# Optimization experiments

Measured on AMD Instinct MI355X. Metric: run time of the kernel, lower is better.

The kernel has to match this reference:

```python
import jax, jax.numpy as jnp
import numpy as np

A, B, T, N, C = 8, 4, 1024, 4, 2048
EPS = 1e-5
SINKHORN_ITERS = 20


def setup_inputs() -> dict:
    key = jax.random.key(0)
    ks = jax.random.split(key, 8)
    nC = N * C
    # identity-ish init per module, with small random alphas to exercise all paths
    p = 1.0 / N
    inv_sig = float(np.log(p) - np.log(1.0 - p))
    return {
        "x": jax.random.normal(ks[0], (B, T, N, C), dtype=jnp.float32),
        "output": jax.random.normal(ks[1], (B, T, C), dtype=jnp.float32),
        "input_norm_weight": jnp.ones((A, nC), dtype=jnp.float32),
        "phi_pre": 0.02 * jax.random.normal(ks[2], (A, nC, N), dtype=jnp.float32),
        "phi_post": 0.02 * jax.random.normal(ks[3], (A, nC, N), dtype=jnp.float32),
        "phi_res": 0.02 * jax.random.normal(ks[4], (A, nC, N * N), dtype=jnp.float32),
        "b_pre": jnp.full((A, N), inv_sig, dtype=jnp.float32),
        "b_post": jnp.zeros((A, N), dtype=jnp.float32),
        "b_res": jnp.broadcast_to(10.0 * jnp.eye(N, dtype=jnp.float32), (A, N, N)),
        "alpha_pre": 0.1 * jax.random.normal(ks[5], (A,), dtype=jnp.float32),
        "alpha_post": 0.1 * jax.random.normal(ks[6], (A,), dtype=jnp.float32),
        "alpha_res": 0.1 * jax.random.normal(ks[7], (A,), dtype=jnp.float32),
        "adapter_indices": jax.random.randint(jax.random.fold_in(key, 99), (B,), 0, A, dtype=jnp.int32),
    }


def sinkhorn_knopp(logits, iters):
    # logits: (B,T,n,n) -> doubly-stochastic M via alternating row/col normalization
    M = jnp.exp(logits)
    for _ in range(iters):
        M = M / M.sum(axis=-1, keepdims=True)
        M = M / M.sum(axis=-2, keepdims=True)
    return M


def reference(x, output, input_norm_weight, phi_pre, phi_post, phi_res,
              b_pre, b_post, b_res, alpha_pre, alpha_post, alpha_res,
              adapter_indices):
    Bs, Ts, n, Cc = x.shape
    idx = adapter_indices
    # per-sample adapter gather
    w = input_norm_weight[idx]                      # (B, n*C)
    x_flat = x.reshape(Bs, Ts, n * Cc)              # (B, T, n*C)
    rms = jnp.sqrt(jnp.mean(x_flat * x_flat, axis=-1, keepdims=True) + EPS)
    x_norm = w[:, None, :] * x_flat / rms           # (B, T, n*C)
    # pre gating
    pre_logits = jnp.einsum('btf,bfn->btn', x_norm, phi_pre[idx])
    H_pre = jax.nn.sigmoid(alpha_pre[idx][:, None, None] * pre_logits + b_pre[idx][:, None, :])
    x_agg = jnp.einsum('btn,btnc->btc', H_pre, x)   # (B, T, C)
    # post gating
    post_logits = jnp.einsum('btf,bfn->btn', x_norm, phi_post[idx])
    H_post = 2.0 * jax.nn.sigmoid(alpha_post[idx][:, None, None] * post_logits + b_post[idx][:, None, :])
    # residual mixing matrix via Sinkhorn
    res_logits = jnp.einsum('btf,bfm->btm', x_norm, phi_res[idx]).reshape(Bs, Ts, n, n)
    tilde_res = alpha_res[idx][:, None, None, None] * res_logits + b_res[idx][:, None, :, :]
    M = sinkhorn_knopp(tilde_res, SINKHORN_ITERS)   # (B, T, n, n)
    x_mixed = jnp.einsum('btij,btjc->btic', M, x)   # (B, T, n, C)
    y_dist = H_post[..., None] * output[:, :, None, :]
    out = x_mixed + y_dist                          # (B, T, n, C)
    return x_agg, out
```

## Files before the change

kernel.cpp:

```cpp
#include <hip/hip_runtime.h>

#define EPS 1e-5f
#define TOKS 4096
#define NCF 8192
#define CCH 2048
#define PHI_T_BYTES ((size_t)8 * 32 * 8192 * 2)
#define GATES_OFF PHI_T_BYTES
#define WS_NEED (PHI_T_BYTES + (size_t)TOKS * 32 * 4)

typedef __attribute__((ext_vector_type(8))) short bf16x8;
typedef __attribute__((ext_vector_type(4))) float f32x4;

__device__ __forceinline__ unsigned short f2bf(float f) {
  unsigned int u = __float_as_uint(f);
  u += 0x7FFFu + ((u >> 16) & 1u);
  return (unsigned short)(u >> 16);
}
__device__ __forceinline__ float bf2f(unsigned short s) {
  return __uint_as_float(((unsigned int)s) << 16);
}

__global__ __launch_bounds__(256)
void prep_phiT(const float* __restrict__ pre, const float* __restrict__ post,
               const float* __restrict__ res, unsigned short* __restrict__ phiT) {
  const int gid = blockIdx.x * 256 + threadIdx.x;
  const int a = gid >> 15;
  const int r = (gid >> 10) & 31;
  const int f = (gid & 1023) * 8;
  unsigned int w[4];
  #pragma unroll
  for (int p = 0; p < 4; ++p) {
    float v0 = 0.f, v1 = 0.f;
    const int e0 = f + 2 * p, e1 = f + 2 * p + 1;
    if (r < 4) {
      v0 = pre[((size_t)a * NCF + e0) * 4 + r];
      v1 = pre[((size_t)a * NCF + e1) * 4 + r];
    } else if (r < 8) {
      v0 = post[((size_t)a * NCF + e0) * 4 + (r - 4)];
      v1 = post[((size_t)a * NCF + e1) * 4 + (r - 4)];
    } else if (r < 24) {
      v0 = res[((size_t)a * NCF + e0) * 16 + (r - 8)];
      v1 = res[((size_t)a * NCF + e1) * 16 + (r - 8)];
    }
    w[p] = (unsigned int)f2bf(v0) | ((unsigned int)f2bf(v1) << 16);
  }
  *(uint4*)(phiT + ((size_t)a * 32 + r) * NCF + f) = make_uint4(w[0], w[1], w[2], w[3]);
}

__global__ __launch_bounds__(512, 1)
void logits_gates(const float* __restrict__ x,
                  const float* __restrict__ wnorm,
                  const unsigned short* __restrict__ phiT,
                  const float* __restrict__ b_pre, const float* __restrict__ b_post,
                  const float* __restrict__ b_res,
                  const float* __restrict__ a_pre, const float* __restrict__ a_post,
                  const float* __restrict__ a_res,
                  const int* __restrict__ aidx_arr,
                  float* __restrict__ gates) {
  __shared__ unsigned short xs[8][16 * 264];
  __shared__ float logits_s[8][16][32];
  __shared__ float ssq_s[8][16];

  const int tid = threadIdx.x;
  const int wave = tid >> 6, lane = tid & 63;
  const int tok0 = blockIdx.x * 16;
  const int aidx = aidx_arr[tok0 >> 10];
  const int kbase = wave * 1024;

  const float* xbase = x + (size_t)tok0 * NCF + kbase + lane * 4;
  const float* wbase = wnorm + (size_t)aidx * NCF + kbase + lane * 4;
  const unsigned short* pBbase =
      phiT + ((size_t)aidx * 32 + (lane & 15)) * NCF + kbase + (lane >> 4) * 8;

  f32x4 acc0 = {0.f, 0.f, 0.f, 0.f};
  f32x4 acc1 = {0.f, 0.f, 0.f, 0.f};
  float ssq[16];
  #pragma unroll
  for (int r = 0; r < 16; ++r) ssq[r] = 0.f;

  float4 xr[16];
  #pragma unroll
  for (int r = 0; r < 16; ++r) xr[r] = *(const float4*)(xbase + (size_t)r * NCF);

  for (int t = 0; t < 4; ++t) {
    const float4 wv = *(const float4*)(wbase + t * 256);
    #pragma unroll
    for (int r = 0; r < 16; ++r) {
      const float4 xv = xr[r];
      ssq[r] += xv.x * xv.x + xv.y * xv.y + xv.z * xv.z + xv.w * xv.w;
      ushort4 u = make_ushort4(f2bf(xv.x * wv.x), f2bf(xv.y * wv.y),
                               f2bf(xv.z * wv.z), f2bf(xv.w * wv.w));
      *(ushort4*)&xs[wave][r * 264 + lane * 4] = u;
    }
    if (t < 3) {
      #pragma unroll
      for (int r = 0; r < 16; ++r)
        xr[r] = *(const float4*)(xbase + (size_t)r * NCF + (t + 1) * 256);
    }
    const unsigned short* pB = pBbase + t * 256;
    #pragma unroll
    for (int s = 0; s < 8; ++s) {
      bf16x8 a = *(const bf16x8*)&xs[wave][(lane & 15) * 264 + s * 32 + (lane >> 4) * 8];
      bf16x8 b0 = *(const bf16x8*)(pB + s * 32);
      bf16x8 b1 = *(const bf16x8*)(pB + 16 * NCF + s * 32);
      acc0 = __builtin_amdgcn_mfma_f32_16x16x32_bf16(a, b0, acc0, 0, 0, 0);
      acc1 = __builtin_amdgcn_mfma_f32_16x16x32_bf16(a, b1, acc1, 0, 0, 0);
    }
  }

  #pragma unroll
  for (int r = 0; r < 16; ++r) {
    float v = ssq[r];
    #pragma unroll
    for (int m = 1; m <= 32; m <<= 1) v += __shfl_xor(v, m, 64);
    if (lane == 0) ssq_s[wave][r] = v;
  }
  #pragma unroll
  for (int i = 0; i < 4; ++i) {
    logits_s[wave][(lane >> 4) * 4 + i][lane & 15] = acc0[i];
    logits_s[wave][(lane >> 4) * 4 + i][16 + (lane & 15)] = acc1[i];
  }
  __syncthreads();

  if (tid < 256) {
    const int tok = tid >> 4, cl = tid & 15;
    float L0 = 0.f, L16 = 0.f, ssqt = 0.f;
    #pragma unroll
    for (int w = 0; w < 8; ++w) {
      L0 += logits_s[w][tok][cl];
      L16 += logits_s[w][tok][16 + cl];
      ssqt += ssq_s[w][tok];
    }
    const float invr = rsqrtf(ssqt * (1.f / NCF) + EPS);

    float* g = gates + (size_t)(tok0 + tok) * 32;
    if (cl < 4) {
      const float zp = a_pre[aidx] * L0 * invr + b_pre[(size_t)aidx * 4 + cl];
      g[cl] = 1.f / (1.f + __expf(-zp));
    } else if (cl < 8) {
      const float zq = a_post[aidx] * L0 * invr + b_post[(size_t)aidx * 4 + (cl - 4)];
      g[cl] = 2.f / (1.f + __expf(-zq));
    }
    const float resv = __shfl_xor((cl & 8) ? L0 : L16, 8, 64);
    const float tl = a_res[aidx] * resv * invr + b_res[(size_t)aidx * 16 + cl];
    float m = __expf(tl);
    #pragma unroll
    for (int it = 0; it < 20; ++it) {
      float rs = m;
      rs += __shfl_xor(rs, 1, 64);
      rs += __shfl_xor(rs, 2, 64);
      m *= __builtin_amdgcn_rcpf(rs);
      float cs = m;
      cs += __shfl_xor(cs, 4, 64);
      cs += __shfl_xor(cs, 8, 64);
      m *= __builtin_amdgcn_rcpf(cs);
    }
    g[8 + cl] = m;
  }
}

__global__ __launch_bounds__(256)
void out_pass(const float* __restrict__ x, const float* __restrict__ outp,
              const float* __restrict__ gates,
              float* __restrict__ agg, float* __restrict__ big) {
  const int tok = blockIdx.x;
  const int tid = threadIdx.x;
  const float* g = gates + (size_t)tok * 32;
  float hp[4], hq[4], M[16];
  #pragma unroll
  for (int i = 0; i < 4; ++i) { hp[i] = g[i]; hq[i] = g[4 + i]; }
  #pragma unroll
  for (int i = 0; i < 16; ++i) M[i] = g[8 + i];

  const float* xrow = x + (size_t)tok * NCF;
  const float* orow = outp + (size_t)tok * CCH;
  float* arow = agg + (size_t)tok * CCH;
  float* brow = big + (size_t)tok * NCF;

  #pragma unroll
  for (int rep = 0; rep < 2; ++rep) {
    const int c = rep * 1024 + tid * 4;
    float4 xv[4];
    #pragma unroll
    for (int j = 0; j < 4; ++j) xv[j] = *(const float4*)(xrow + j * CCH + c);
    const float4 ov = *(const float4*)(orow + c);

    f32x4 ag;
    ag.x = hp[0]*xv[0].x + hp[1]*xv[1].x + hp[2]*xv[2].x + hp[3]*xv[3].x;
    ag.y = hp[0]*xv[0].y + hp[1]*xv[1].y + hp[2]*xv[2].y + hp[3]*xv[3].y;
    ag.z = hp[0]*xv[0].z + hp[1]*xv[1].z + hp[2]*xv[2].z + hp[3]*xv[3].z;
    ag.w = hp[0]*xv[0].w + hp[1]*xv[1].w + hp[2]*xv[2].w + hp[3]*xv[3].w;
    __builtin_nontemporal_store(ag, (f32x4*)(arow + c));

    #pragma unroll
    for (int i = 0; i < 4; ++i) {
      const float m0 = M[i*4+0], m1 = M[i*4+1], m2 = M[i*4+2], m3 = M[i*4+3];
      f32x4 o;
      o.x = m0*xv[0].x + m1*xv[1].x + m2*xv[2].x + m3*xv[3].x + hq[i]*ov.x;
      o.y = m0*xv[0].y + m1*xv[1].y + m2*xv[2].y + m3*xv[3].y + hq[i]*ov.y;
      o.z = m0*xv[0].z + m1*xv[1].z + m2*xv[2].z + m3*xv[3].z + hq[i]*ov.z;
      o.w = m0*xv[0].w + m1*xv[1].w + m2*xv[2].w + m3*xv[3].w + hq[i]*ov.w;
      __builtin_nontemporal_store(o, (f32x4*)(brow + i * CCH + c));
    }
  }
}

__global__ __launch_bounds__(256, 4)
void lora_fused(const float* __restrict__ x, const float* __restrict__ outp,
                const float* __restrict__ wnorm, const float* __restrict__ phi_pre,
                const float* __restrict__ phi_post, const float* __restrict__ phi_res,
                const float* __restrict__ b_pre, const float* __restrict__ b_post,
                const float* __restrict__ b_res, const float* __restrict__ a_pre,
                const float* __restrict__ a_post, const float* __restrict__ a_res,
                const int* __restrict__ aidx_arr, float* __restrict__ agg_out,
                float* __restrict__ big_out) {
  __shared__ unsigned short xsb[2][NCF];
  __shared__ float scratch[4][52];
  __shared__ float red[52];
  __shared__ float Hpre[2][4], Hpost[2][4], Msm[2][16];
  const int tid = threadIdx.x;
  const int tok0 = blockIdx.x * 2;
  const int aidx = aidx_arr[tok0 >> 10];
  const float* xr0 = x + (size_t)tok0 * NCF;
  const float* xr1 = xr0 + NCF;
  const float* wr = wnorm + (size_t)aidx * NCF;
  const float* pp = phi_pre + (size_t)aidx * NCF * 4;
  const float* pq = phi_post + (size_t)aidx * NCF * 4;
  const float* pr = phi_res + (size_t)aidx * NCF * 16;
  float acc[50];
  #pragma unroll
  for (int i = 0; i < 50; ++i) acc[i] = 0.f;
  for (int k = 0; k < 8; ++k) {
    const int f0 = (k * 256 + tid) * 4;
    const float4 w4 = *(const float4*)(wr + f0);
    const float4 xa = *(const float4*)(xr0 + f0);
    const float4 xb = *(const float4*)(xr1 + f0);
    acc[0] += xa.x*xa.x + xa.y*xa.y + xa.z*xa.z + xa.w*xa.w;
    acc[25] += xb.x*xb.x + xb.y*xb.y + xb.z*xb.z + xb.w*xb.w;
    float xw0[4] = { xa.x*w4.x, xa.y*w4.y, xa.z*w4.z, xa.w*w4.w };
    float xw1[4] = { xb.x*w4.x, xb.y*w4.y, xb.z*w4.z, xb.w*w4.w };
    *(ushort4*)&xsb[0][f0] = make_ushort4(f2bf(xa.x), f2bf(xa.y), f2bf(xa.z), f2bf(xa.w));
    *(ushort4*)&xsb[1][f0] = make_ushort4(f2bf(xb.x), f2bf(xb.y), f2bf(xb.z), f2bf(xb.w));
    #pragma unroll
    for (int d = 0; d < 4; ++d) {
      const int f = f0 + d;
      const float a0 = xw0[d], a1 = xw1[d];
      float col[24];
      const float4 P = *(const float4*)(pp + ((size_t)f << 2));
      const float4 Q = *(const float4*)(pq + ((size_t)f << 2));
      const float4 R0 = *(const float4*)(pr + ((size_t)f << 4));
      const float4 R1 = *(const float4*)(pr + ((size_t)f << 4) + 4);
      const float4 R2 = *(const float4*)(pr + ((size_t)f << 4) + 8);
      const float4 R3 = *(const float4*)(pr + ((size_t)f << 4) + 12);
      col[0]=P.x; col[1]=P.y; col[2]=P.z; col[3]=P.w;
      col[4]=Q.x; col[5]=Q.y; col[6]=Q.z; col[7]=Q.w;
      col[8]=R0.x; col[9]=R0.y; col[10]=R0.z; col[11]=R0.w;
      col[12]=R1.x; col[13]=R1.y; col[14]=R1.z; col[15]=R1.w;
      col[16]=R2.x; col[17]=R2.y; col[18]=R2.z; col[19]=R2.w;
      col[20]=R3.x; col[21]=R3.y; col[22]=R3.z; col[23]=R3.w;
      #pragma unroll
      for (int c = 0; c < 24; ++c) { acc[1 + c] += a0 * col[c]; acc[26 + c] += a1 * col[c]; }
    }
  }
  #pragma unroll
  for (int m = 1; m <= 32; m <<= 1) {
    #pragma unroll
    for (int v = 0; v < 50; ++v) acc[v] += __shfl_xor(acc[v], m, 64);
  }
  const int wave = tid >> 6, lane = tid & 63;
  if (lane == 0) {
    #pragma unroll
    for (int v = 0; v < 50; ++v) scratch[wave][v] = acc[v];
  }
  __syncthreads();
  if (tid < 50) red[tid] = scratch[0][tid] + scratch[1][tid] + scratch[2][tid] + scratch[3][tid];
  __syncthreads();
  if (tid < 32) {
    const int t = tid >> 4, l = tid & 15;
    const float invr = rsqrtf(red[t * 25] * (1.f / NCF) + EPS);
    const float tl = a_res[aidx] * red[t * 25 + 1 + 8 + l] * invr + b_res[(size_t)aidx * 16 + l];
    float m = __expf(tl);
    #pragma unroll
    for (int it = 0; it < 20; ++it) {
      float rs = m; rs += __shfl_xor(rs, 1, 64); rs += __shfl_xor(rs, 2, 64);
      m *= __builtin_amdgcn_rcpf(rs);
      float cs = m; cs += __shfl_xor(cs, 4, 64); cs += __shfl_xor(cs, 8, 64);
      m *= __builtin_amdgcn_rcpf(cs);
    }
    Msm[t][l] = m;
  } else if (tid < 40) {
    const int q = tid - 32, t = q >> 2, n = q & 3;
    const float invr = rsqrtf(red[t * 25] * (1.f / NCF) + EPS);
    const float zp = a_pre[aidx] * red[t * 25 + 1 + n] * invr + b_pre[(size_t)aidx * 4 + n];
    const float zq = a_post[aidx] * red[t * 25 + 1 + 4 + n] * invr + b_post[(size_t)aidx * 4 + n];
    Hpre[t][n] = 1.f / (1.f + __expf(-zp));
    Hpost[t][n] = 2.f / (1.f + __expf(-zq));
  }
  __syncthreads();
  #pragma unroll
  for (int t = 0; t < 2; ++t) {
    const int tok = tok0 + t;
    const float* orow = outp + (size_t)tok * CCH;
    float* arow = agg_out + (size_t)tok * CCH;
    float* brow = big_out + (size_t)tok * 4 * CCH;
    const float hp0 = Hpre[t][0], hp1 = Hpre[t][1], hp2 = Hpre[t][2], hp3 = Hpre[t][3];
    float Mr[16];
    #pragma unroll
    for (int i = 0; i < 16; ++i) Mr[i] = Msm[t][i];
    const float hq[4] = { Hpost[t][0], Hpost[t][1], Hpost[t][2], Hpost[t][3] };
    #pragma unroll
    for (int w = 0; w < 2; ++w) {
      const int c0 = (w * 256 + tid) * 4;
      float4 xv[4];
      #pragma unroll
      for (int n = 0; n < 4; ++n) {
        const ushort4 u = *(const ushort4*)&xsb[t][n * CCH + c0];
        xv[n] = make_float4(bf2f(u.x), bf2f(u.y), bf2f(u.z), bf2f(u.w));
      }
      const float4 ov = *(const float4*)(orow + c0);
      float4 ag;
      ag.x = hp0*xv[0].x + hp1*xv[1].x + hp2*xv[2].x + hp3*xv[3].x;
      ag.y = hp0*xv[0].y + hp1*xv[1].y + hp2*xv[2].y + hp3*xv[3].y;
      ag.z = hp0*xv[0].z + hp1*xv[1].z + hp2*xv[2].z + hp3*xv[3].z;
      ag.w = hp0*xv[0].w + hp1*xv[1].w + hp2*xv[2].w + hp3*xv[3].w;
      *(float4*)(arow + c0) = ag;
      #pragma unroll
      for (int i = 0; i < 4; ++i) {
        const float m0 = Mr[i*4+0], m1 = Mr[i*4+1], m2 = Mr[i*4+2], m3 = Mr[i*4+3];
        float4 o;
        o.x = m0*xv[0].x + m1*xv[1].x + m2*xv[2].x + m3*xv[3].x + hq[i]*ov.x;
        o.y = m0*xv[0].y + m1*xv[1].y + m2*xv[2].y + m3*xv[3].y + hq[i]*ov.y;
        o.z = m0*xv[0].z + m1*xv[1].z + m2*xv[2].z + m3*xv[3].z + hq[i]*ov.z;
        o.w = m0*xv[0].w + m1*xv[1].w + m2*xv[2].w + m3*xv[3].w + hq[i]*ov.w;
        *(float4*)(brow + (size_t)i * CCH + c0) = o;
      }
    }
  }
}

extern "C" void kernel_launch(void* const* d_in, const int* in_sizes, int n_in,
                              void* d_out, int out_size, void* d_ws, size_t ws_size,
                              hipStream_t stream) {
  const float* x     = (const float*)d_in[0];
  const float* outp  = (const float*)d_in[1];
  const float* wnorm = (const float*)d_in[2];
  const float* ppre  = (const float*)d_in[3];
  const float* ppost = (const float*)d_in[4];
  const float* pres  = (const float*)d_in[5];
  const float* bpre  = (const float*)d_in[6];
  const float* bpost = (const float*)d_in[7];
  const float* bres  = (const float*)d_in[8];
  const float* apre  = (const float*)d_in[9];
  const float* apost = (const float*)d_in[10];
  const float* ares  = (const float*)d_in[11];
  const int*   aidx  = (const int*)d_in[12];

  float* agg = (float*)d_out;
  float* big = (float*)d_out + (size_t)TOKS * CCH;

  if (ws_size >= WS_NEED) {
    unsigned short* phiT = (unsigned short*)d_ws;
    float* gates = (float*)((char*)d_ws + GATES_OFF);
    hipLaunchKernelGGL(prep_phiT, dim3(1024), dim3(256), 0, stream, ppre, ppost, pres, phiT);
    hipLaunchKernelGGL(logits_gates, dim3(256), dim3(512), 0, stream,
                       x, wnorm, phiT, bpre, bpost, bres, apre, apost, ares, aidx, gates);
    hipLaunchKernelGGL(out_pass, dim3(4096), dim3(256), 0, stream, x, outp, gates, agg, big);
  } else {
    hipLaunchKernelGGL(lora_fused, dim3(2048), dim3(256), 0, stream,
                       x, outp, wnorm, ppre, ppost, pres,
                       bpre, bpost, bres, apre, apost, ares, aidx, agg, big);
  }
}
```

Measured before the change: 100.7 us.

## Fuse gate computation and output pass, keep x tile in registers as bf16

Merges the logits/gates kernel and the output kernel into one kernel, so x is read from global memory once instead of twice. The gates stay in shared memory. Each thread keeps its x slice as packed bf16 in registers and reuses it for the aggregate and mixed outputs. The RMS-norm weight is folded into the transposed phi during prep, and waves now split the work by channel slice across the four streams. The cost is lower output precision (x is rounded to bf16 before mixing), heavy register pressure with possible spills, and only one large block per CU during the store-heavy phase.

After: 159.6 us. 58.5% more time.

```diff
diff --git a/kernel.cpp b/kernel.cpp
--- a/kernel.cpp
+++ b/kernel.cpp
@@ -4,9 +4,7 @@
 #define TOKS 4096
 #define NCF 8192
 #define CCH 2048
-#define PHI_T_BYTES ((size_t)8 * 32 * 8192 * 2)
-#define GATES_OFF PHI_T_BYTES
-#define WS_NEED (PHI_T_BYTES + (size_t)TOKS * 32 * 4)
+#define WS_NEED ((size_t)8 * 32 * 8192 * 2)
 
 typedef __attribute__((ext_vector_type(8))) short bf16x8;
 typedef __attribute__((ext_vector_type(4))) float f32x4;
@@ -22,11 +20,15 @@
 
 __global__ __launch_bounds__(256)
 void prep_phiT(const float* __restrict__ pre, const float* __restrict__ post,
-               const float* __restrict__ res, unsigned short* __restrict__ phiT) {
+               const float* __restrict__ res, const float* __restrict__ wnorm,
+               unsigned short* __restrict__ phiT) {
   const int gid = blockIdx.x * 256 + threadIdx.x;
   const int a = gid >> 15;
   const int r = (gid >> 10) & 31;
   const int f = (gid & 1023) * 8;
+  const float4 wA = *(const float4*)(wnorm + (size_t)a * NCF + f);
+  const float4 wB = *(const float4*)(wnorm + (size_t)a * NCF + f + 4);
+  const float wv[8] = { wA.x, wA.y, wA.z, wA.w, wB.x, wB.y, wB.z, wB.w };
   unsigned int w[4];
   #pragma unroll
   for (int p = 0; p < 4; ++p) {
@@ -42,35 +44,37 @@
       v0 = res[((size_t)a * NCF + e0) * 16 + (r - 8)];
       v1 = res[((size_t)a * NCF + e1) * 16 + (r - 8)];
     }
+    v0 *= wv[2 * p];
+    v1 *= wv[2 * p + 1];
     w[p] = (unsigned int)f2bf(v0) | ((unsigned int)f2bf(v1) << 16);
   }
   *(uint4*)(phiT + ((size_t)a * 32 + r) * NCF + f) = make_uint4(w[0], w[1], w[2], w[3]);
 }
 
-__global__ __launch_bounds__(512, 1)
-void logits_gates(const float* __restrict__ x,
-                  const float* __restrict__ wnorm,
+__global__ __launch_bounds__(512)
+void lora_fused16(const float* __restrict__ x,
+                  const float* __restrict__ outp,
                   const unsigned short* __restrict__ phiT,
                   const float* __restrict__ b_pre, const float* __restrict__ b_post,
                   const float* __restrict__ b_res,
                   const float* __restrict__ a_pre, const float* __restrict__ a_post,
                   const float* __restrict__ a_res,
                   const int* __restrict__ aidx_arr,
-                  float* __restrict__ gates) {
+                  float* __restrict__ agg, float* __restrict__ big) {
   __shared__ unsigned short xs[8][16 * 264];
   __shared__ float logits_s[8][16][32];
   __shared__ float ssq_s[8][16];
+  __shared__ float gates_s[16][24];
 
   const int tid = threadIdx.x;
   const int wave = tid >> 6, lane = tid & 63;
   const int tok0 = blockIdx.x * 16;
   const int aidx = aidx_arr[tok0 >> 10];
-  const int kbase = wave * 1024;
-
-  const float* xbase = x + (size_t)tok0 * NCF + kbase + lane * 4;
-  const float* wbase = wnorm + (size_t)aidx * NCF + kbase + lane * 4;
+  const int cbase = wave * 256 + lane * 4;
+
+  const float* xbase = x + (size_t)tok0 * NCF + cbase;
   const unsigned short* pBbase =
-      phiT + ((size_t)aidx * 32 + (lane & 15)) * NCF + kbase + (lane >> 4) * 8;
+      phiT + ((size_t)aidx * 32 + (lane & 15)) * NCF + wave * 256 + (lane >> 4) * 8;
 
   f32x4 acc0 = {0.f, 0.f, 0.f, 0.f};
   f32x4 acc1 = {0.f, 0.f, 0.f, 0.f};
@@ -78,26 +82,28 @@
   #pragma unroll
   for (int r = 0; r < 16; ++r) ssq[r] = 0.f;
 
+  uint2 xsav[16][4];
+
   float4 xr[16];
   #pragma unroll
   for (int r = 0; r < 16; ++r) xr[r] = *(const float4*)(xbase + (size_t)r * NCF);
 
-  for (int t = 0; t < 4; ++t) {
-    const float4 wv = *(const float4*)(wbase + t * 256);
+  for (int n = 0; n < 4; ++n) {
     #pragma unroll
     for (int r = 0; r < 16; ++r) {
-      const float4 xv = xr[r];
-      ssq[r] += xv.x * xv.x + xv.y * xv.y + xv.z * xv.z + xv.w * xv.w;
-      ushort4 u = make_ushort4(f2bf(xv.x * wv.x), f2bf(xv.y * wv.y),
-                               f2bf(xv.z * wv.z), f2bf(xv.w * wv.w));
-      *(ushort4*)&xs[wave][r * 264 + lane * 4] = u;
-    }
-    if (t < 3) {
+      const float4 v = xr[r];
+      ssq[r] += v.x * v.x + v.y * v.y + v.z * v.z + v.w * v.w;
+      const unsigned int lo = (unsigned int)f2bf(v.x) | ((unsigned int)f2bf(v.y) << 16);
+      const unsigned int hi = (unsigned int)f2bf(v.z) | ((unsigned int)f2bf(v.w) << 16);
+      xsav[r][n] = make_uint2(lo, hi);
+      *(uint2*)&xs[wave][r * 264 + lane * 4] = make_uint2(lo, hi);
+    }
+    if (n < 3) {
       #pragma unroll
       for (int r = 0; r < 16; ++r)
-        xr[r] = *(const float4*)(xbase + (size_t)r * NCF + (t + 1) * 256);
-    }
-    const unsigned short* pB = pBbase + t * 256;
+        xr[r] = *(const float4*)(xbase + (size_t)r * NCF + (n + 1) * 2048);
+    }
+    const unsigned short* pB = pBbase + n * 2048;
     #pragma unroll
     for (int s = 0; s < 8; ++s) {
       bf16x8 a = *(const bf16x8*)&xs[wave][(lane & 15) * 264 + s * 32 + (lane >> 4) * 8];
@@ -133,13 +139,12 @@
     }
     const float invr = rsqrtf(ssqt * (1.f / NCF) + EPS);
 
-    float* g = gates + (size_t)(tok0 + tok) * 32;
     if (cl < 4) {
       const float zp = a_pre[aidx] * L0 * invr + b_pre[(size_t)aidx * 4 + cl];
-      g[cl] = 1.f / (1.f + __expf(-zp));
+      gates_s[tok][cl] = 1.f / (1.f + __expf(-zp));
     } else if (cl < 8) {
       const float zq = a_post[aidx] * L0 * invr + b_post[(size_t)aidx * 4 + (cl - 4)];
-      g[cl] = 2.f / (1.f + __expf(-zq));
+      gates_s[tok][cl] = 2.f / (1.f + __expf(-zq));
     }
     const float resv = __shfl_xor((cl & 8) ? L0 : L16, 8, 64);
     const float tl = a_res[aidx] * resv * invr + b_res[(size_t)aidx * 16 + cl];
@@ -155,52 +160,48 @@
       cs += __shfl_xor(cs, 8, 64);
       m *= __builtin_amdgcn_rcpf(cs);
     }
-    g[8 + cl] = m;
-  }
-}
-
-__global__ __launch_bounds__(256)
-void out_pass(const float* __restrict__ x, const float* __restrict__ outp,
-              const float* __restrict__ gates,
-              float* __restrict__ agg, float* __restrict__ big) {
-  const int tok = blockIdx.x;
-  const int tid = threadIdx.x;
-  const float* g = gates + (size_t)tok * 32;
-  float hp[4], hq[4], M[16];
-  #pragma unroll
-  for (int i = 0; i < 4; ++i) { hp[i] = g[i]; hq[i] = g[4 + i]; }
-  #pragma unroll
-  for (int i = 0; i < 16; ++i) M[i] = g[8 + i];
-
-  const float* xrow = x + (size_t)tok * NCF;
-  const float* orow = outp + (size_t)tok * CCH;
-  float* arow = agg + (size_t)tok * CCH;
-  float* brow = big + (size_t)tok * NCF;
-
-  #pragma unroll
-  for (int rep = 0; rep < 2; ++rep) {
-    const int c = rep * 1024 + tid * 4;
-    float4 xv[4];
-    #pragma unroll
-    for (int j = 0; j < 4; ++j) xv[j] = *(const float4*)(xrow + j * CCH + c);
-    const float4 ov = *(const float4*)(orow + c);
+    gates_s[tok][8 + cl] = m;
+  }
+  __syncthreads();
+
+  #pragma unroll
+  for (int r = 0; r < 16; ++r) {
+    const int gtok = tok0 + r;
+    const float hp0 = gates_s[r][0], hp1 = gates_s[r][1],
+                hp2 = gates_s[r][2], hp3 = gates_s[r][3];
+    const float hq[4] = { gates_s[r][4], gates_s[r][5], gates_s[r][6], gates_s[r][7] };
+    float M[16];
+    #pragma unroll
+    for (int i = 0; i < 16; ++i) M[i] = gates_s[r][8 + i];
+
+    float4 xw[4];
+    #pragma unroll
+    for (int j = 0; j < 4; ++j) {
+      const uint2 p = xsav[r][j];
+      xw[j] = make_float4(bf2f((unsigned short)(p.x & 0xffff)),
+                          bf2f((unsigned short)(p.x >> 16)),
+                          bf2f((unsigned short)(p.y & 0xffff)),
+                          bf2f((unsigned short)(p.y >> 16)));
+    }
+    const float4 ov = *(const float4*)(outp + (size_t)gtok * CCH + cbase);
 
     f32x4 ag;
-    ag.x = hp[0]*xv[0].x + hp[1]*xv[1].x + hp[2]*xv[2].x + hp[3]*xv[3].x;
-    ag.y = hp[0]*xv[0].y + hp[1]*xv[1].y + hp[2]*xv[2].y + hp[3]*xv[3].y;
-    ag.z = hp[0]*xv[0].z + hp[1]*xv[1].z + hp[2]*xv[2].z + hp[3]*xv[3].z;
-    ag.w = hp[0]*xv[0].w + hp[1]*xv[1].w + hp[2]*xv[2].w + hp[3]*xv[3].w;
-    __builtin_nontemporal_store(ag, (f32x4*)(arow + c));
-
+    ag.x = hp0*xw[0].x + hp1*xw[1].x + hp2*xw[2].x + hp3*xw[3].x;
+    ag.y = hp0*xw[0].y + hp1*xw[1].y + hp2*xw[2].y + hp3*xw[3].y;
+    ag.z = hp0*xw[0].z + hp1*xw[1].z + hp2*xw[2].z + hp3*xw[3].z;
+    ag.w = hp0*xw[0].w + hp1*xw[1].w + hp2*xw[2].w + hp3*xw[3].w;
+    __builtin_nontemporal_store(ag, (f32x4*)(agg + (size_t)gtok * CCH + cbase));
+
+    float* brow = big + (size_t)gtok * NCF + cbase;
     #pragma unroll
     for (int i = 0; i < 4; ++i) {
       const float m0 = M[i*4+0], m1 = M[i*4+1], m2 = M[i*4+2], m3 = M[i*4+3];
       f32x4 o;
-      o.x = m0*xv[0].x + m1*xv[1].x + m2*xv[2].x + m3*xv[3].x + hq[i]*ov.x;
-      o.y = m0*xv[0].y + m1*xv[1].y + m2*xv[2].y + m3*xv[3].y + hq[i]*ov.y;
-      o.z = m0*xv[0].z + m1*xv[1].z + m2*xv[2].z + m3*xv[3].z + hq[i]*ov.z;
-      o.w = m0*xv[0].w + m1*xv[1].w + m2*xv[2].w + m3*xv[3].w + hq[i]*ov.w;
-      __builtin_nontemporal_store(o, (f32x4*)(brow + i * CCH + c));
+      o.x = m0*xw[0].x + m1*xw[1].x + m2*xw[2].x + m3*xw[3].x + hq[i]*ov.x;
+      o.y = m0*xw[0].y + m1*xw[1].y + m2*xw[2].y + m3*xw[3].y + hq[i]*ov.y;
+      o.z = m0*xw[0].z + m1*xw[1].z + m2*xw[2].z + m3*xw[3].z + hq[i]*ov.z;
+      o.w = m0*xw[0].w + m1*xw[1].w + m2*xw[2].w + m3*xw[3].w + hq[i]*ov.w;
+      __builtin_nontemporal_store(o, (f32x4*)(brow + (size_t)i * CCH));
     }
   }
 }
@@ -360,11 +361,10 @@
 
   if (ws_size >= WS_NEED) {
     unsigned short* phiT = (unsigned short*)d_ws;
-    float* gates = (float*)((char*)d_ws + GATES_OFF);
-    hipLaunchKernelGGL(prep_phiT, dim3(1024), dim3(256), 0, stream, ppre, ppost, pres, phiT);
-    hipLaunchKernelGGL(logits_gates, dim3(256), dim3(512), 0, stream,
-                       x, wnorm, phiT, bpre, bpost, bres, apre, apost, ares, aidx, gates);
-    hipLaunchKernelGGL(out_pass, dim3(4096), dim3(256), 0, stream, x, outp, gates, agg, big);
+    hipLaunchKernelGGL(prep_phiT, dim3(1024), dim3(256), 0, stream,
+                       ppre, ppost, pres, wnorm, phiT);
+    hipLaunchKernelGGL(lora_fused16, dim3(256), dim3(512), 0, stream,
+                       x, outp, phiT, bpre, bpost, bres, apre, apost, ares, aidx, agg, big);
   } else {
     hipLaunchKernelGGL(lora_fused, dim3(2048), dim3(256), 0, stream,
                        x, outp, wnorm, ppre, ppost, pres,
```

## Split logits GEMM over K into two blocks and fold norm weight into phi

Applied to the files above, without the earlier changes.

The logits kernel is split into two blocks per 16-token tile, each covering half of the feature dimension. Each block writes partial logits and sum-of-squares to workspace, and a new small kernel reduces them and computes the gates and Sinkhorn. The per-adapter RMSNorm weight is premultiplied into the bf16 phi matrix during prep, which removes a load and multiply from the hot loop. This doubles the grid and allows higher occupancy, at the cost of an extra launch and a workspace round trip for the partials.

Measured after the change: 149.8 us. 48.7% more time.

```diff
diff --git a/kernel.cpp b/kernel.cpp
--- a/kernel.cpp
+++ b/kernel.cpp
@@ -4,9 +4,12 @@
 #define TOKS 4096
 #define NCF 8192
 #define CCH 2048
-#define PHI_T_BYTES ((size_t)8 * 32 * 8192 * 2)
-#define GATES_OFF PHI_T_BYTES
-#define WS_NEED (PHI_T_BYTES + (size_t)TOKS * 32 * 4)
+
+#define PHI_BYTES ((size_t)8 * 32 * 8192 * 2)
+#define LOGP_OFF  PHI_BYTES
+#define SSQP_OFF  (LOGP_OFF + (size_t)512 * 16 * 32 * 4)
+#define GATES_OFF (SSQP_OFF + (size_t)512 * 16 * 4)
+#define WS_NEED   (GATES_OFF + (size_t)TOKS * 32 * 4)
 
 typedef __attribute__((ext_vector_type(8))) short bf16x8;
 typedef __attribute__((ext_vector_type(4))) float f32x4;
@@ -22,11 +25,15 @@
 
 __global__ __launch_bounds__(256)
 void prep_phiT(const float* __restrict__ pre, const float* __restrict__ post,
-               const float* __restrict__ res, unsigned short* __restrict__ phiT) {
+               const float* __restrict__ res, const float* __restrict__ wnorm,
+               unsigned short* __restrict__ phiT) {
   const int gid = blockIdx.x * 256 + threadIdx.x;
   const int a = gid >> 15;
   const int r = (gid >> 10) & 31;
   const int f = (gid & 1023) * 8;
+  const float4 wA = *(const float4*)(wnorm + (size_t)a * NCF + f);
+  const float4 wB = *(const float4*)(wnorm + (size_t)a * NCF + f + 4);
+  const float wv[8] = { wA.x, wA.y, wA.z, wA.w, wB.x, wB.y, wB.z, wB.w };
   unsigned int w[4];
   #pragma unroll
   for (int p = 0; p < 4; ++p) {
@@ -42,121 +49,129 @@
       v0 = res[((size_t)a * NCF + e0) * 16 + (r - 8)];
       v1 = res[((size_t)a * NCF + e1) * 16 + (r - 8)];
     }
+    v0 *= wv[2 * p];
+    v1 *= wv[2 * p + 1];
     w[p] = (unsigned int)f2bf(v0) | ((unsigned int)f2bf(v1) << 16);
   }
   *(uint4*)(phiT + ((size_t)a * 32 + r) * NCF + f) = make_uint4(w[0], w[1], w[2], w[3]);
 }
 
-__global__ __launch_bounds__(512, 1)
-void logits_gates(const float* __restrict__ x,
-                  const float* __restrict__ wnorm,
-                  const unsigned short* __restrict__ phiT,
+__global__ __launch_bounds__(512, 4)
+void logits_partial(const float* __restrict__ x,
+                    const unsigned short* __restrict__ phiT,
+                    const int* __restrict__ aidx_arr,
+                    float* __restrict__ logP,
+                    float* __restrict__ ssqP) {
+  __shared__ unsigned short xs[8][16 * 264];
+  __shared__ float logAcc[16][32];
+  __shared__ float ssqAcc[16];
+
+  const int tid = threadIdx.x;
+  const int wave = tid >> 6, lane = tid & 63;
+  const int tile = blockIdx.x >> 1;
+  const int h = blockIdx.x & 1;
+  const int tok0 = tile * 16;
+  const int koff = h * 4096;
+  const int aidx = aidx_arr[tok0 >> 10];
+
+  if (tid < 512) logAcc[tid >> 5][tid & 31] = 0.f;
+  if (tid < 16) ssqAcc[tid] = 0.f;
+  __syncthreads();
+
+  const float* xbase = x + (size_t)tok0 * NCF + koff + wave * 512 + lane * 4;
+  const unsigned short* pBbase =
+      phiT + ((size_t)aidx * 32 + (lane & 15)) * NCF + koff + wave * 512 + (lane >> 4) * 8;
+
+  f32x4 acc0 = {0.f, 0.f, 0.f, 0.f};
+  f32x4 acc1 = {0.f, 0.f, 0.f, 0.f};
+  float ssq[16];
+  #pragma unroll
+  for (int r = 0; r < 16; ++r) ssq[r] = 0.f;
+
+  for (int t = 0; t < 2; ++t) {
+    float4 xv[16];
+    #pragma unroll
+    for (int r = 0; r < 16; ++r)
+      xv[r] = *(const float4*)(xbase + (size_t)r * NCF + t * 256);
+    #pragma unroll
+    for (int r = 0; r < 16; ++r) {
+      const float4 v = xv[r];
+      ssq[r] += v.x * v.x + v.y * v.y + v.z * v.z + v.w * v.w;
+      *(ushort4*)&xs[wave][r * 264 + lane * 4] =
+          make_ushort4(f2bf(v.x), f2bf(v.y), f2bf(v.z), f2bf(v.w));
+    }
+    const unsigned short* pB = pBbase + t * 256;
+    #pragma unroll
+    for (int s = 0; s < 8; ++s) {
+      bf16x8 a = *(const bf16x8*)&xs[wave][(lane & 15) * 264 + s * 32 + (lane >> 4) * 8];
+      bf16x8 b0 = *(const bf16x8*)(pB + s * 32);
+      bf16x8 b1 = *(const bf16x8*)(pB + 16 * NCF + s * 32);
+      acc0 = __builtin_amdgcn_mfma_f32_16x16x32_bf16(a, b0, acc0, 0, 0, 0);
+      acc1 = __builtin_amdgcn_mfma_f32_16x16x32_bf16(a, b1, acc1, 0, 0, 0);
+    }
+  }
+
+  #pragma unroll
+  for (int r = 0; r < 16; ++r) {
+    float v = ssq[r];
+    #pragma unroll
+    for (int m = 1; m <= 32; m <<= 1) v += __shfl_xor(v, m, 64);
+    if (lane == 0) atomicAdd(&ssqAcc[r], v);
+  }
+  #pragma unroll
+  for (int i = 0; i < 4; ++i) {
+    atomicAdd(&logAcc[(lane >> 4) * 4 + i][lane & 15], acc0[i]);
+    atomicAdd(&logAcc[(lane >> 4) * 4 + i][16 + (lane & 15)], acc1[i]);
+  }
+  __syncthreads();
+
+  if (tid < 512) logP[(size_t)blockIdx.x * 512 + tid] = logAcc[tid >> 5][tid & 31];
+  if (tid < 16) ssqP[(size_t)blockIdx.x * 16 + tid] = ssqAcc[tid];
+}
+
+__global__ __launch_bounds__(256)
+void gates_kernel(const float* __restrict__ logP, const float* __restrict__ ssqP,
                   const float* __restrict__ b_pre, const float* __restrict__ b_post,
                   const float* __restrict__ b_res,
                   const float* __restrict__ a_pre, const float* __restrict__ a_post,
                   const float* __restrict__ a_res,
                   const int* __restrict__ aidx_arr,
                   float* __restrict__ gates) {
-  __shared__ unsigned short xs[8][16 * 264];
-  __shared__ float logits_s[8][16][32];
-  __shared__ float ssq_s[8][16];
-
+  const int tile = blockIdx.x;
   const int tid = threadIdx.x;
-  const int wave = tid >> 6, lane = tid & 63;
-  const int tok0 = blockIdx.x * 16;
+  const int tok = tid >> 4, cl = tid & 15;
+  const int tok0 = tile * 16;
   const int aidx = aidx_arr[tok0 >> 10];
-  const int kbase = wave * 1024;
-
-  const float* xbase = x + (size_t)tok0 * NCF + kbase + lane * 4;
-  const float* wbase = wnorm + (size_t)aidx * NCF + kbase + lane * 4;
-  const unsigned short* pBbase =
-      phiT + ((size_t)aidx * 32 + (lane & 15)) * NCF + kbase + (lane >> 4) * 8;
-
-  f32x4 acc0 = {0.f, 0.f, 0.f, 0.f};
-  f32x4 acc1 = {0.f, 0.f, 0.f, 0.f};
-  float ssq[16];
-  #pragma unroll
-  for (int r = 0; r < 16; ++r) ssq[r] = 0.f;
-
-  float4 xr[16];
-  #pragma unroll
-  for (int r = 0; r < 16; ++r) xr[r] = *(const float4*)(xbase + (size_t)r * NCF);
-
-  for (int t = 0; t < 4; ++t) {
-    const float4 wv = *(const float4*)(wbase + t * 256);
-    #pragma unroll
-    for (int r = 0; r < 16; ++r) {
-      const float4 xv = xr[r];
-      ssq[r] += xv.x * xv.x + xv.y * xv.y + xv.z * xv.z + xv.w * xv.w;
-      ushort4 u = make_ushort4(f2bf(xv.x * wv.x), f2bf(xv.y * wv.y),
-                               f2bf(xv.z * wv.z), f2bf(xv.w * wv.w));
-      *(ushort4*)&xs[wave][r * 264 + lane * 4] = u;
-    }
-    if (t < 3) {
-      #pragma unroll
-      for (int r = 0; r < 16; ++r)
-        xr[r] = *(const float4*)(xbase + (size_t)r * NCF + (t + 1) * 256);
-    }
-    const unsigned short* pB = pBbase + t * 256;
-    #pragma unroll
-    for (int s = 0; s < 8; ++s) {
-      bf16x8 a = *(const bf16x8*)&xs[wave][(lane & 15) * 264 + s * 32 + (lane >> 4) * 8];
-      bf16x8 b0 = *(const bf16x8*)(pB + s * 32);
-      bf16x8 b1 = *(const bf16x8*)(pB + 16 * NCF + s * 32);
-      acc0 = __builtin_amdgcn_mfma_f32_16x16x32_bf16(a, b0, acc0, 0, 0, 0);
-      acc1 = __builtin_amdgcn_mfma_f32_16x16x32_bf16(a, b1, acc1, 0, 0, 0);
-    }
-  }
-
-  #pragma unroll
-  for (int r = 0; r < 16; ++r) {
-    float v = ssq[r];
-    #pragma unroll
-    for (int m = 1; m <= 32; m <<= 1) v += __shfl_xor(v, m, 64);
-    if (lane == 0) ssq_s[wave][r] = v;
-  }
-  #pragma unroll
-  for (int i = 0; i < 4; ++i) {
-    logits_s[wave][(lane >> 4) * 4 + i][lane & 15] = acc0[i];
-    logits_s[wave][(lane >> 4) * 4 + i][16 + (lane & 15)] = acc1[i];
-  }
-  __syncthreads();
-
-  if (tid < 256) {
-    const int tok = tid >> 4, cl = tid & 15;
-    float L0 = 0.f, L16 = 0.f, ssqt = 0.f;
-    #pragma unroll
-    for (int w = 0; w < 8; ++w) {
-      L0 += logits_s[w][tok][cl];
-      L16 += logits_s[w][tok][16 + cl];
-      ssqt += ssq_s[w][tok];
-    }
-    const float invr = rsqrtf(ssqt * (1.f / NCF) + EPS);
-
-    float* g = gates + (size_t)(tok0 + tok) * 32;
-    if (cl < 4) {
-      const float zp = a_pre[aidx] * L0 * invr + b_pre[(size_t)aidx * 4 + cl];
-      g[cl] = 1.f / (1.f + __expf(-zp));
-    } else if (cl < 8) {
-      const float zq = a_post[aidx] * L0 * invr + b_post[(size_t)aidx * 4 + (cl - 4)];
-      g[cl] = 2.f / (1.f + __expf(-zq));
-    }
-    const float resv = __shfl_xor((cl & 8) ? L0 : L16, 8, 64);
-    const float tl = a_res[aidx] * resv * invr + b_res[(size_t)aidx * 16 + cl];
-    float m = __expf(tl);
-    #pragma unroll
-    for (int it = 0; it < 20; ++it) {
-      float rs = m;
-      rs += __shfl_xor(rs, 1, 64);
-      rs += __shfl_xor(rs, 2, 64);
-      m *= __builtin_amdgcn_rcpf(rs);
-      float cs = m;
-      cs += __shfl_xor(cs, 4, 64);
-      cs += __shfl_xor(cs, 8, 64);
-      m *= __builtin_amdgcn_rcpf(cs);
-    }
-    g[8 + cl] = m;
-  }
+
+  const float* p0 = logP + (size_t)(tile * 2) * 512 + tok * 32;
+  const float* p1 = logP + (size_t)(tile * 2 + 1) * 512 + tok * 32;
+  const float Lg   = p0[cl] + p1[cl];
+  const float Lres = p0[8 + cl] + p1[8 + cl];
+  const float ssqt = ssqP[(size_t)(tile * 2) * 16 + tok] + ssqP[(size_t)(tile * 2 + 1) * 16 + tok];
+  const float invr = rsqrtf(ssqt * (1.f / NCF) + EPS);
+
+  float* g = gates + (size_t)(tok0 + tok) * 32;
+  if (cl < 4) {
+    const float zp = a_pre[aidx] * Lg * invr + b_pre[(size_t)aidx * 4 + cl];
+    g[cl] = 1.f / (1.f + __expf(-zp));
+  } else if (cl < 8) {
+    const float zq = a_post[aidx] * Lg * invr + b_post[(size_t)aidx * 4 + (cl - 4)];
+    g[cl] = 2.f / (1.f + __expf(-zq));
+  }
+  const float tl = a_res[aidx] * Lres * invr + b_res[(size_t)aidx * 16 + cl];
+  float m = __expf(tl);
+  #pragma unroll
+  for (int it = 0; it < 20; ++it) {
+    float rs = m;
+    rs += __shfl_xor(rs, 1, 64);
+    rs += __shfl_xor(rs, 2, 64);
+    m *= __builtin_amdgcn_rcpf(rs);
+    float cs = m;
+    cs += __shfl_xor(cs, 4, 64);
+    cs += __shfl_xor(cs, 8, 64);
+    m *= __builtin_amdgcn_rcpf(cs);
+  }
+  g[8 + cl] = m;
 }
 
 __global__ __launch_bounds__(256)
@@ -360,10 +375,15 @@
 
   if (ws_size >= WS_NEED) {
     unsigned short* phiT = (unsigned short*)d_ws;
+    float* logP  = (float*)((char*)d_ws + LOGP_OFF);
+    float* ssqP  = (float*)((char*)d_ws + SSQP_OFF);
     float* gates = (float*)((char*)d_ws + GATES_OFF);
-    hipLaunchKernelGGL(prep_phiT, dim3(1024), dim3(256), 0, stream, ppre, ppost, pres, phiT);
-    hipLaunchKernelGGL(logits_gates, dim3(256), dim3(512), 0, stream,
-                       x, wnorm, phiT, bpre, bpost, bres, apre, apost, ares, aidx, gates);
+    hipLaunchKernelGGL(prep_phiT, dim3(1024), dim3(256), 0, stream,
+                       ppre, ppost, pres, wnorm, phiT);
+    hipLaunchKernelGGL(logits_partial, dim3(512), dim3(512), 0, stream,
+                       x, phiT, aidx, logP, ssqP);
+    hipLaunchKernelGGL(gates_kernel, dim3(256), dim3(256), 0, stream,
+                       logP, ssqP, bpre, bpost, bres, apre, apost, ares, aidx, gates);
     hipLaunchKernelGGL(out_pass, dim3(4096), dim3(256), 0, stream, x, outp, gates, agg, big);
   } else {
     hipLaunchKernelGGL(lora_fused, dim3(2048), dim3(256), 0, stream,
```

## Fold norm weight into phi prep and double-buffer x loads in logits kernel

Applied to the files above, without the earlier changes.

Moves the per-adapter norm weight multiplication into the phi transpose prep kernel, so the logits kernel no longer loads wnorm or multiplies x by it. The logits kernel now keeps two register buffers of x tiles, prefetching two K-steps ahead with the loop fully unrolled. Launch bounds are raised to allow two blocks per CU. The extra register buffer may raise register pressure against the tighter occupancy bound, and the bf16 rounding point moves to the weight-scaled phi.

Measured after the change: 110.5 us. 9.6% more time.

```diff
diff --git a/kernel.cpp b/kernel.cpp
--- a/kernel.cpp
+++ b/kernel.cpp
@@ -4,9 +4,10 @@
 #define TOKS 4096
 #define NCF 8192
 #define CCH 2048
-#define PHI_T_BYTES ((size_t)8 * 32 * 8192 * 2)
-#define GATES_OFF PHI_T_BYTES
-#define WS_NEED (PHI_T_BYTES + (size_t)TOKS * 32 * 4)
+
+#define PHI_BYTES ((size_t)8 * 32 * 8192 * 2)
+#define GATES_OFF PHI_BYTES
+#define WS_NEED   (GATES_OFF + (size_t)TOKS * 32 * 4)
 
 typedef __attribute__((ext_vector_type(8))) short bf16x8;
 typedef __attribute__((ext_vector_type(4))) float f32x4;
@@ -22,11 +23,15 @@
 
 __global__ __launch_bounds__(256)
 void prep_phiT(const float* __restrict__ pre, const float* __restrict__ post,
-               const float* __restrict__ res, unsigned short* __restrict__ phiT) {
+               const float* __restrict__ res, const float* __restrict__ wnorm,
+               unsigned short* __restrict__ phiT) {
   const int gid = blockIdx.x * 256 + threadIdx.x;
   const int a = gid >> 15;
   const int r = (gid >> 10) & 31;
   const int f = (gid & 1023) * 8;
+  const float4 wA = *(const float4*)(wnorm + (size_t)a * NCF + f);
+  const float4 wB = *(const float4*)(wnorm + (size_t)a * NCF + f + 4);
+  const float wv[8] = { wA.x, wA.y, wA.z, wA.w, wB.x, wB.y, wB.z, wB.w };
   unsigned int w[4];
   #pragma unroll
   for (int p = 0; p < 4; ++p) {
@@ -42,14 +47,15 @@
       v0 = res[((size_t)a * NCF + e0) * 16 + (r - 8)];
       v1 = res[((size_t)a * NCF + e1) * 16 + (r - 8)];
     }
+    v0 *= wv[2 * p];
+    v1 *= wv[2 * p + 1];
     w[p] = (unsigned int)f2bf(v0) | ((unsigned int)f2bf(v1) << 16);
   }
   *(uint4*)(phiT + ((size_t)a * 32 + r) * NCF + f) = make_uint4(w[0], w[1], w[2], w[3]);
 }
 
-__global__ __launch_bounds__(512, 1)
+__global__ __launch_bounds__(512, 2)
 void logits_gates(const float* __restrict__ x,
-                  const float* __restrict__ wnorm,
                   const unsigned short* __restrict__ phiT,
                   const float* __restrict__ b_pre, const float* __restrict__ b_post,
                   const float* __restrict__ b_res,
@@ -68,7 +74,6 @@
   const int kbase = wave * 1024;
 
   const float* xbase = x + (size_t)tok0 * NCF + kbase + lane * 4;
-  const float* wbase = wnorm + (size_t)aidx * NCF + kbase + lane * 4;
   const unsigned short* pBbase =
       phiT + ((size_t)aidx * 32 + (lane & 15)) * NCF + kbase + (lane >> 4) * 8;
 
@@ -78,24 +83,24 @@
   #pragma unroll
   for (int r = 0; r < 16; ++r) ssq[r] = 0.f;
 
-  float4 xr[16];
-  #pragma unroll
-  for (int r = 0; r < 16; ++r) xr[r] = *(const float4*)(xbase + (size_t)r * NCF);
-
+  float4 xa[16], xb[16];
+  #pragma unroll
+  for (int r = 0; r < 16; ++r) xa[r] = *(const float4*)(xbase + (size_t)r * NCF);
+  #pragma unroll
+  for (int r = 0; r < 16; ++r) xb[r] = *(const float4*)(xbase + (size_t)r * NCF + 256);
+
+  #pragma unroll
   for (int t = 0; t < 4; ++t) {
-    const float4 wv = *(const float4*)(wbase + t * 256);
     #pragma unroll
     for (int r = 0; r < 16; ++r) {
-      const float4 xv = xr[r];
-      ssq[r] += xv.x * xv.x + xv.y * xv.y + xv.z * xv.z + xv.w * xv.w;
-      ushort4 u = make_ushort4(f2bf(xv.x * wv.x), f2bf(xv.y * wv.y),
-                               f2bf(xv.z * wv.z), f2bf(xv.w * wv.w));
-      *(ushort4*)&xs[wave][r * 264 + lane * 4] = u;
-    }
-    if (t < 3) {
-      #pragma unroll
-      for (int r = 0; r < 16; ++r)
-        xr[r] = *(const float4*)(xbase + (size_t)r * NCF + (t + 1) * 256);
+      const float4 v = (t & 1) ? xb[r] : xa[r];
+      ssq[r] += v.x * v.x + v.y * v.y + v.z * v.z + v.w * v.w;
+      *(ushort4*)&xs[wave][r * 264 + lane * 4] =
+          make_ushort4(f2bf(v.x), f2bf(v.y), f2bf(v.z), f2bf(v.w));
+      if (t < 2) {
+        const float4 nv = *(const float4*)(xbase + (size_t)r * NCF + (t + 2) * 256);
+        if (t & 1) xb[r] = nv; else xa[r] = nv;
+      }
     }
     const unsigned short* pB = pBbase + t * 256;
     #pragma unroll
@@ -361,9 +366,10 @@
   if (ws_size >= WS_NEED) {
     unsigned short* phiT = (unsigned short*)d_ws;
     float* gates = (float*)((char*)d_ws + GATES_OFF);
-    hipLaunchKernelGGL(prep_phiT, dim3(1024), dim3(256), 0, stream, ppre, ppost, pres, phiT);
+    hipLaunchKernelGGL(prep_phiT, dim3(1024), dim3(256), 0, stream,
+                       ppre, ppost, pres, wnorm, phiT);
     hipLaunchKernelGGL(logits_gates, dim3(256), dim3(512), 0, stream,
-                       x, wnorm, phiT, bpre, bpost, bres, apre, apost, ares, aidx, gates);
+                       x, phiT, bpre, bpost, bres, apre, apost, ares, aidx, gates);
     hipLaunchKernelGGL(out_pass, dim3(4096), dim3(256), 0, stream, x, outp, gates, agg, big);
   } else {
     hipLaunchKernelGGL(lora_fused, dim3(2048), dim3(256), 0, stream,
```
